# Kernel tuning notes

Hardware: AMD Instinct MI355X
Metric: run time of the kernel (lower is better)

The kernel has to match this reference:

```python
import jax, jax.numpy as jnp
import numpy as np

K, D, O, B = 65536, 256, 256, 1024

def setup_inputs() -> dict:
    key = jax.random.key(0)
    k1, k2, k3 = jax.random.split(key, 3)
    return {
        "x": jax.random.normal(k1, (B, D), dtype=jnp.float32),
        "mean": jax.random.normal(k2, (K, D), dtype=jnp.float32),
        "stddev": jnp.ones((K, D), dtype=jnp.float32),
        "outputs": jax.random.normal(k3, (K, O), dtype=jnp.float32),
        "top_k": 32,
    }

def reference(x, mean, stddev, outputs, top_k):
    # Joint Gaussian log-prob summed over feature dim, computed without the
    # [B, K, D] broadcast torch materializes. Expanding sum_d ((x-mu)/sigma)^2
    # gives three GEMM-shaped terms.
    d = x.shape[-1]
    inv_var = 1.0 / (stddev * stddev)                      # [K, D]
    quad = ((x * x) @ inv_var.T                            # [B, K]
            - 2.0 * (x @ (mean * inv_var).T)
            + jnp.sum(mean * mean * inv_var, axis=-1))
    log_norm = jnp.sum(jnp.log(stddev), axis=-1) + 0.5 * d * jnp.log(2.0 * jnp.pi)
    joint_lp = -0.5 * quad - log_norm                      # [B, K]
    top_lp, top_idx = jax.lax.top_k(joint_lp, top_k)       # [B, top_k]
    weights = jax.nn.softmax(top_lp, axis=-1)              # [B, top_k]
    gathered = outputs[top_idx]                            # [B, top_k, O]
    return jnp.einsum('bko,bk->bo', gathered, weights)     # [B, O]
```

## Files before the change

kernel.cpp:

```cpp
#include <hip/hip_runtime.h>
#include <stdint.h>

#define KCOMP 65536
#define DDIM  256
#define ODIM  256
#define BROWS 1024
#define NCB   512
#define NBLK  1024
#define LOG2PI_TERM 235.2482645f

typedef float f32x4 __attribute__((ext_vector_type(4)));
typedef __bf16 bf16x8 __attribute__((ext_vector_type(8)));
typedef unsigned int u32;
typedef unsigned long long u64;
typedef unsigned short u16;

typedef __attribute__((address_space(1))) const u32 gconst_u32;
typedef __attribute__((address_space(3))) u32 lds_u32;

__device__ __forceinline__ u16 f2bf(float f) {
  u32 b = __float_as_uint(f);
  b += 0x7FFFu + ((b >> 16) & 1u);
  return (u16)(b >> 16);
}
__device__ __forceinline__ u32 fkey(float f) {
  u32 b = __float_as_uint(f);
  return b ^ ((b >> 31) ? 0xFFFFFFFFu : 0x80000000u);
}

#define DPP_ROR1 0x121
#define DPP_ROR2 0x122
#define DPP_ROR4 0x124
#define DPP_ROR8 0x128

#define WS_A     0
#define WS_W     (1u << 20)
#define WS_CONST (WS_W + (64u << 20))
#define WS_KEY   (WS_CONST + (256u << 10))

__global__ void prep_A(const float* __restrict__ x, u16* __restrict__ A) {
  int l = threadIdx.x & 63;
  int wv = threadIdx.x >> 6;
  int t = blockIdx.x;
  int row = t * 16 + (l & 15);
  for (int u = 0; u < 4; ++u) {
    int cc = wv * 4 + u;
    int d0 = cc * 16 + ((l >> 4) << 2);
    float4 xv = *(const float4*)(x + (size_t)row * DDIM + d0);
    float xs[4] = {xv.x, xv.y, xv.z, xv.w};
    uint4 v;
    u32 wds[4];
    for (int e = 0; e < 4; ++e)
      wds[e] = (u32)f2bf(xs[e] * xs[e]) | ((u32)f2bf(-2.0f * xs[e]) << 16);
    v.x = wds[0]; v.y = wds[1]; v.z = wds[2]; v.w = wds[3];
    *(uint4*)(A + ((size_t)(t * 16 + cc) * 64 + l) * 8) = v;
  }
}

__global__ __launch_bounds__(256)
void prep_W(const float* __restrict__ mean, const float* __restrict__ stdd,
            u16* __restrict__ W, float* __restrict__ ck) {
  __shared__ u32 ldsW[4][16][268];
  int l = threadIdx.x & 63;
  int wv = threadIdx.x >> 6;
  int g = blockIdx.x * 4 + wv;
  for (int p = 0; p < 16; ++p) {
    int comp = g * 16 + p;
    float4 m4 = *(const float4*)(mean + (size_t)comp * DDIM + l * 4);
    float4 s4 = *(const float4*)(stdd + (size_t)comp * DDIM + l * 4);
    float ms[4] = {m4.x, m4.y, m4.z, m4.w};
    float ss[4] = {s4.x, s4.y, s4.z, s4.w};
    u32 wds[4];
    float gsum = 0.f;
    for (int e = 0; e < 4; ++e) {
      float iv = 1.0f / (ss[e] * ss[e]);
      float miv = ms[e] * iv;
      wds[e] = (u32)f2bf(iv) | ((u32)f2bf(miv) << 16);
      gsum += -0.5f * ms[e] * miv - __logf(ss[e]);
    }
    for (int d = 1; d < 64; d <<= 1) gsum += __shfl_xor(gsum, d);
    if (l == 0) ck[comp] = gsum - LOG2PI_TERM;
    uint4 v; v.x = wds[0]; v.y = wds[1]; v.z = wds[2]; v.w = wds[3];
    *(uint4*)&ldsW[wv][p][l * 4] = v;
  }
  __syncthreads();
  for (int cc = 0; cc < 16; ++cc) {
    uint4 v = *(const uint4*)&ldsW[wv][l & 15][cc * 16 + ((l >> 4) << 2)];
    *(uint4*)(W + ((size_t)(g * 16 + cc) * 64 + l) * 8) = v;
  }
}

__global__ __launch_bounds__(256, 2)
void main_gemm(const u16* __restrict__ A_ws, const u16* __restrict__ W_ws,
               const float* __restrict__ ck, u32* __restrict__ ckey) {
  __shared__ u16 Ash[2][16][512];
  __shared__ u32 wsel[2][16][9];
  int tid = threadIdx.x, l = tid & 63, w = tid >> 6;
  int nb = blockIdx.x & (NCB - 1);
  int rh = blockIdx.x >> 9;
  int g0 = nb * 8 + w * 2;

  bf16x8 wfA[16], wfB[16];
#pragma unroll
  for (int cc = 0; cc < 16; ++cc) {
    wfA[cc] = *(const bf16x8*)(W_ws + ((size_t)(g0 * 16 + cc) * 64 + l) * 8);
    wfB[cc] = *(const bf16x8*)(W_ws + ((size_t)((g0 + 1) * 16 + cc) * 64 + l) * 8);
  }
  float mycA = ck[g0 * 16 + (l & 15)];
  float mycB = ck[(g0 + 1) * 16 + (l & 15)];
  u32 cA = (u32)(w * 32 + (l & 15));
  u32 cB = cA + 16;

#define ISSUE(S, B)                                                           \
  {                                                                           \
    _Pragma("unroll")                                                         \
    for (int u = 0; u < 4; ++u) {                                             \
      int cell = w * 4 + u;                                                   \
      const u16* gsrc = A_ws +                                                \
        ((size_t)(rh * 32 + (S)) * 16 + cell) * 512 + (size_t)l * 8;          \
      __builtin_amdgcn_global_load_lds((gconst_u32*)gsrc,                     \
          (lds_u32*)&Ash[B][cell][0], 16, 0, 0);                              \
    }                                                                         \
  }

#define MERGE_EMIT(ST, B)                                                     \
  {                                                                           \
    int r = tid;                                                              \
    u32 top[4] = {~0u, ~0u, ~0u, ~0u};                                        \
    _Pragma("unroll")                                                         \
    for (int j = 0; j < 8; ++j) {                                             \
      u32 key = wsel[B][r][j];                                                \
      if (key < top[3]) {                                                     \
        top[3] = key;                                                         \
        for (int z = 3; z > 0 && top[z] < top[z - 1]; --z) {                  \
          u32 tt = top[z]; top[z] = top[z - 1]; top[z - 1] = tt;              \
        }                                                                     \
      }                                                                       \
    }                                                                         \
    int rowg = rh * 512 + (ST) * 16 + r;                                      \
    uint4 ov; ov.x = ~top[0]; ov.y = ~top[1]; ov.z = ~top[2]; ov.w = ~top[3]; \
    *(uint4*)&ckey[((size_t)rowg * NCB + nb) * 4] = ov;                       \
  }

  ISSUE(0, 0)
  for (int s = 0; s < 32; ++s) {
    int p = s & 1;
    __syncthreads();
    if (s < 31) ISSUE(s + 1, p ^ 1)
    if (s > 0 && tid < 16) MERGE_EMIT(s - 1, p ^ 1)

    f32x4 aA = (f32x4){0.f, 0.f, 0.f, 0.f};
    f32x4 aB = (f32x4){0.f, 0.f, 0.f, 0.f};
#pragma unroll
    for (int cc = 0; cc < 16; ++cc) {
      bf16x8 a = *(const bf16x8*)(&Ash[p][cc][(size_t)l * 8]);
      aA = __builtin_amdgcn_mfma_f32_16x16x32_bf16(a, wfA[cc], aA, 0, 0, 0);
      aB = __builtin_amdgcn_mfma_f32_16x16x32_bf16(a, wfB[cc], aB, 0, 0, 0);
    }

#pragma unroll
    for (int i = 0; i < 4; ++i) {
      float sA = fmaf(aA[i], -0.5f, mycA);
      float sB = fmaf(aB[i], -0.5f, mycB);
      u32 kA = (__float_as_uint(sA) & 0xFFFFFF00u) | cA;
      u32 kB = (__float_as_uint(sB) & 0xFFFFFF00u) | cB;
      u32 m1 = kA < kB ? kA : kB;
      u32 m2 = kA < kB ? kB : kA;
#define DSTEP(CTRL)                                                           \
      {                                                                       \
        u32 o1 = (u32)__builtin_amdgcn_mov_dpp((int)m1, CTRL, 0xf, 0xf, false); \
        u32 o2 = (u32)__builtin_amdgcn_mov_dpp((int)m2, CTRL, 0xf, 0xf, false); \
        u32 lo = m1 < o1 ? m1 : o1;                                           \
        u32 hi = m1 < o1 ? o1 : m1;                                           \
        u32 mn = m2 < o2 ? m2 : o2;                                           \
        m2 = hi < mn ? hi : mn;                                               \
        m1 = lo;                                                              \
      }
      DSTEP(DPP_ROR1) DSTEP(DPP_ROR2) DSTEP(DPP_ROR4) DSTEP(DPP_ROR8)
#undef DSTEP
      int r = ((l >> 4) << 2) + i;
      if ((l & 15) == 0) wsel[p][r][w * 2] = m1;
      else if ((l & 15) == 1) wsel[p][r][w * 2 + 1] = m2;
    }
  }
  __syncthreads();
  if (tid < 16) MERGE_EMIT(31, 1)
#undef ISSUE
#undef MERGE_EMIT
}

__global__ __launch_bounds__(256)
void finalize(const float* __restrict__ x, const float* __restrict__ mean,
              const float* __restrict__ stdd, const float* __restrict__ outs,
              const u32* __restrict__ ckey, float* __restrict__ out) {
  __shared__ u32 cksh[2048];
  __shared__ float xr[256];
  __shared__ float part[256];
  __shared__ int selk[64];
  __shared__ float ew[32];
  __shared__ int kf[32];
  __shared__ float invs_sh;
  int tid = threadIdx.x, l = tid & 63, v = tid >> 6;
  int row = blockIdx.x;

  for (int i = tid; i < 2048; i += 256)
    cksh[i] = ckey[(size_t)row * 2048 + i];
  xr[tid] = x[(size_t)row * DDIM + tid];
  __syncthreads();

#define REDUCE_MAX(m)                                                         \
  {                                                                           \
    u32 o;                                                                    \
    o = (u32)__builtin_amdgcn_mov_dpp((int)m, DPP_ROR1, 0xf, 0xf, false);     \
    m = m > o ? m : o;                                                        \
    o = (u32)__builtin_amdgcn_mov_dpp((int)m, DPP_ROR2, 0xf, 0xf, false);     \
    m = m > o ? m : o;                                                        \
    o = (u32)__builtin_amdgcn_mov_dpp((int)m, DPP_ROR4, 0xf, 0xf, false);     \
    m = m > o ? m : o;                                                        \
    o = (u32)__builtin_amdgcn_mov_dpp((int)m, DPP_ROR8, 0xf, 0xf, false);     \
    m = m > o ? m : o;                                                        \
    o = (u32)__shfl_xor((int)m, 16); m = m > o ? m : o;                       \
    o = (u32)__shfl_xor((int)m, 32); m = m > o ? m : o;                       \
  }

  {
    u32 ext[8];
#pragma unroll
    for (int i = 0; i < 8; ++i) {
      int j = v * 512 + i * 64 + l;
      ext[i] = (cksh[j] & 0xFFFFFE00u) | ((u32)l << 3) | (u32)i;
    }
#define CSW(a, b) { if (ext[a] < ext[b]) { u32 t = ext[a]; ext[a] = ext[b]; ext[b] = t; } }
    CSW(0,1) CSW(2,3) CSW(4,5) CSW(6,7)
    CSW(0,2) CSW(1,3) CSW(4,6) CSW(5,7)
    CSW(1,2) CSW(5,6)
    CSW(0,4) CSW(1,5) CSW(2,6) CSW(3,7)
    CSW(2,4) CSW(3,5)
    CSW(1,2) CSW(3,4) CSW(5,6)
#undef CSW
    for (int it = 0; it < 16; ++it) {
      u32 m = ext[0];
      REDUCE_MAX(m)
      if (m == ext[0]) {
#pragma unroll
        for (int z = 0; z < 7; ++z) ext[z] = ext[z + 1];
        ext[7] = 0;
      }
      if (l == 0) {
        int wl = (int)((m >> 3) & 63u), wi = (int)(m & 7u);
        int j = v * 512 + wi * 64 + wl;
        selk[v * 16 + it] = (int)((u32)(j >> 2) * 128u + (~cksh[j] & 0x7Fu));
      }
    }
  }
  __syncthreads();

  {
    int j = tid >> 2, q = tid & 3;
    int k = selk[j];
    const float* mr = mean + (size_t)k * DDIM + q * 64;
    const float* sr = stdd + (size_t)k * DDIM + q * 64;
    float s2 = 0.f, ls = 0.f;
    for (int i = 0; i < 16; ++i) {
      float4 m4 = *(const float4*)(mr + 4 * i);
      float4 s4 = *(const float4*)(sr + 4 * i);
      float4 x4 = *(const float4*)(&xr[q * 64 + 4 * i]);
      { float is = 1.f / s4.x; float df = (x4.x - m4.x) * is; s2 += df * df; ls += __logf(s4.x); }
      { float is = 1.f / s4.y; float df = (x4.y - m4.y) * is; s2 += df * df; ls += __logf(s4.y); }
      { float is = 1.f / s4.z; float df = (x4.z - m4.z) * is; s2 += df * df; ls += __logf(s4.z); }
      { float is = 1.f / s4.w; float df = (x4.w - m4.w) * is; s2 += df * df; ls += __logf(s4.w); }
    }
    part[tid] = -0.5f * s2 - ls;
  }
  __syncthreads();

  if (tid < 64) {
    float lp0 = part[l * 4] + part[l * 4 + 1] + part[l * 4 + 2] +
                part[l * 4 + 3] - LOG2PI_TERM;
    u32 ext = (fkey(lp0) & 0xFFFFFFC0u) | (u32)l;
    float maxlp = 0.f, ssum = 0.f;
    for (int it = 0; it < 32; ++it) {
      u32 m = ext;
      REDUCE_MAX(m)
      int j = (int)(m & 63u);
      u32 vb = m & 0xFFFFFFC0u;
      vb ^= (vb >> 31) ? 0x80000000u : 0xFFFFFFFFu;
      float lp = __uint_as_float(vb);
      if (it == 0) maxlp = lp;
      float e = __expf(lp - maxlp);
      ssum += e;
      if (l == 0) { ew[it] = e; kf[it] = selk[j]; }
      if (j == l) ext = 0;
    }
    if (l == 0) invs_sh = 1.0f / ssum;
  }
  __syncthreads();
#undef REDUCE_MAX

  {
    float a = 0.f;
    for (int i = 0; i < 32; ++i)
      a += ew[i] * outs[(size_t)kf[i] * ODIM + tid];
    out[(size_t)row * ODIM + tid] = a * invs_sh;
  }
}

extern "C" void kernel_launch(void* const* d_in, const int* in_sizes, int n_in,
                              void* d_out, int out_size, void* d_ws, size_t ws_size,
                              hipStream_t stream) {
  const float* x = (const float*)d_in[0];
  const float* mean = (const float*)d_in[1];
  const float* stdd = (const float*)d_in[2];
  const float* outs = (const float*)d_in[3];
  char* ws = (char*)d_ws;
  u16* A_ws = (u16*)(ws + WS_A);
  u16* W_ws = (u16*)(ws + WS_W);
  float* ck = (float*)(ws + WS_CONST);
  u32* ckey = (u32*)(ws + WS_KEY);

  prep_A<<<64, 256, 0, stream>>>(x, A_ws);
  prep_W<<<1024, 256, 0, stream>>>(mean, stdd, W_ws, ck);
  main_gemm<<<NBLK, 256, 0, stream>>>(A_ws, W_ws, ck, ckey);
  finalize<<<BROWS, 256, 0, stream>>>(x, mean, stdd, outs, ckey,
                                      (float*)d_out);
}
```

Baseline: 419.6 us.

## Fuse weight preprocessing into main GEMM and double row tile per stage

Removes the separate prep_W kernel and the bf16 weight workspace. Each main_gemm block now reads mean and stddev directly, builds its bf16 interleaved weight fragments and per-component constants through an LDS scratch area, then runs the GEMM. This avoids writing the intermediate weight buffer and reading it back, at the cost of each component's mean/stddev being read and converted by both row-half blocks. The pipeline also processes 32 rows per stage over 16 stages instead of 16 rows over 32, reusing each weight fragment across two A tiles. That raises LDS use to about 66 KB per block, which may limit occupancy.

```diff
diff --git a/kernel.cpp b/kernel.cpp
--- a/kernel.cpp
+++ b/kernel.cpp
@@ -34,9 +34,7 @@
 #define DPP_ROR8 0x128
 
 #define WS_A     0
-#define WS_W     (1u << 20)
-#define WS_CONST (WS_W + (64u << 20))
-#define WS_KEY   (WS_CONST + (256u << 10))
+#define WS_KEY   (1u << 20)
 
 __global__ void prep_A(const float* __restrict__ x, u16* __restrict__ A) {
   int l = threadIdx.x & 63;
@@ -57,69 +55,68 @@
   }
 }
 
-__global__ __launch_bounds__(256)
-void prep_W(const float* __restrict__ mean, const float* __restrict__ stdd,
-            u16* __restrict__ W, float* __restrict__ ck) {
-  __shared__ u32 ldsW[4][16][268];
-  int l = threadIdx.x & 63;
-  int wv = threadIdx.x >> 6;
-  int g = blockIdx.x * 4 + wv;
-  for (int p = 0; p < 16; ++p) {
-    int comp = g * 16 + p;
-    float4 m4 = *(const float4*)(mean + (size_t)comp * DDIM + l * 4);
-    float4 s4 = *(const float4*)(stdd + (size_t)comp * DDIM + l * 4);
-    float ms[4] = {m4.x, m4.y, m4.z, m4.w};
-    float ss[4] = {s4.x, s4.y, s4.z, s4.w};
-    u32 wds[4];
-    float gsum = 0.f;
-    for (int e = 0; e < 4; ++e) {
-      float iv = 1.0f / (ss[e] * ss[e]);
-      float miv = ms[e] * iv;
-      wds[e] = (u32)f2bf(iv) | ((u32)f2bf(miv) << 16);
-      gsum += -0.5f * ms[e] * miv - __logf(ss[e]);
-    }
-    for (int d = 1; d < 64; d <<= 1) gsum += __shfl_xor(gsum, d);
-    if (l == 0) ck[comp] = gsum - LOG2PI_TERM;
-    uint4 v; v.x = wds[0]; v.y = wds[1]; v.z = wds[2]; v.w = wds[3];
-    *(uint4*)&ldsW[wv][p][l * 4] = v;
-  }
-  __syncthreads();
-  for (int cc = 0; cc < 16; ++cc) {
-    uint4 v = *(const uint4*)&ldsW[wv][l & 15][cc * 16 + ((l >> 4) << 2)];
-    *(uint4*)(W + ((size_t)(g * 16 + cc) * 64 + l) * 8) = v;
-  }
-}
-
 __global__ __launch_bounds__(256, 2)
-void main_gemm(const u16* __restrict__ A_ws, const u16* __restrict__ W_ws,
-               const float* __restrict__ ck, u32* __restrict__ ckey) {
-  __shared__ u16 Ash[2][16][512];
-  __shared__ u32 wsel[2][16][9];
+void main_gemm(const u16* __restrict__ A_ws, const float* __restrict__ mean,
+               const float* __restrict__ stdd, u32* __restrict__ ckey) {
+  __shared__ __align__(16) char lds_raw[66560];
+  __shared__ u32 wsel[2][32][9];
   int tid = threadIdx.x, l = tid & 63, w = tid >> 6;
   int nb = blockIdx.x & (NCB - 1);
   int rh = blockIdx.x >> 9;
   int g0 = nb * 8 + w * 2;
-
-  bf16x8 wfA[16], wfB[16];
-#pragma unroll
-  for (int cc = 0; cc < 16; ++cc) {
-    wfA[cc] = *(const bf16x8*)(W_ws + ((size_t)(g0 * 16 + cc) * 64 + l) * 8);
-    wfB[cc] = *(const bf16x8*)(W_ws + ((size_t)((g0 + 1) * 16 + cc) * 64 + l) * 8);
-  }
-  float mycA = ck[g0 * 16 + (l & 15)];
-  float mycB = ck[(g0 + 1) * 16 + (l & 15)];
-  u32 cA = (u32)(w * 32 + (l & 15));
+  int p = l & 15, q = l >> 4;
+
+  bf16x8 wf[2][16];
+  float myc[2];
+  {
+    u32* scr = (u32*)(lds_raw + w * 16640);
+#pragma unroll
+    for (int gs = 0; gs < 2; ++gs) {
+      int comp = (g0 + gs) * 16 + p;
+      const float* mrow = mean + (size_t)comp * DDIM + q * 64;
+      const float* srow = stdd + (size_t)comp * DDIM + q * 64;
+      float gsum = 0.f;
+#pragma unroll
+      for (int i = 0; i < 16; ++i) {
+        float4 m4 = *(const float4*)(mrow + 4 * i);
+        float4 s4 = *(const float4*)(srow + 4 * i);
+        float ms[4] = {m4.x, m4.y, m4.z, m4.w};
+        float ss[4] = {s4.x, s4.y, s4.z, s4.w};
+        u32 wd[4];
+#pragma unroll
+        for (int e = 0; e < 4; ++e) {
+          float iv = __builtin_amdgcn_rcpf(ss[e] * ss[e]);
+          float miv = ms[e] * iv;
+          wd[e] = (u32)f2bf(iv) | ((u32)f2bf(miv) << 16);
+          gsum -= 0.5f * ms[e] * miv + __logf(ss[e]);
+        }
+        uint4 v; v.x = wd[0]; v.y = wd[1]; v.z = wd[2]; v.w = wd[3];
+        *(uint4*)(scr + p * 260 + q * 64 + i * 4) = v;
+      }
+      gsum += __shfl_xor(gsum, 16);
+      gsum += __shfl_xor(gsum, 32);
+      myc[gs] = gsum - LOG2PI_TERM;
+#pragma unroll
+      for (int cc = 0; cc < 16; ++cc)
+        wf[gs][cc] = *(const bf16x8*)(scr + p * 260 + cc * 16 + q * 4);
+    }
+  }
+  __syncthreads();
+
+  u32 cA = (u32)(w * 32 + p);
   u32 cB = cA + 16;
+#define ASHP(B, CELL) (lds_raw + ((size_t)(B) * 32 + (CELL)) * 1024)
 
 #define ISSUE(S, B)                                                           \
   {                                                                           \
     _Pragma("unroll")                                                         \
-    for (int u = 0; u < 4; ++u) {                                             \
-      int cell = w * 4 + u;                                                   \
+    for (int u = 0; u < 8; ++u) {                                             \
+      int cell = w * 8 + u;                                                   \
       const u16* gsrc = A_ws +                                                \
-        ((size_t)(rh * 32 + (S)) * 16 + cell) * 512 + (size_t)l * 8;          \
+        ((size_t)(rh * 32 + (S) * 2 + (cell >> 4)) * 16 + (cell & 15)) * 512  \
+        + (size_t)l * 8;                                                      \
       __builtin_amdgcn_global_load_lds((gconst_u32*)gsrc,                     \
-          (lds_u32*)&Ash[B][cell][0], 16, 0, 0);                              \
+          (lds_u32*)ASHP(B, cell), 16, 0, 0);                                 \
     }                                                                         \
   }
 
@@ -137,56 +134,66 @@
         }                                                                     \
       }                                                                       \
     }                                                                         \
-    int rowg = rh * 512 + (ST) * 16 + r;                                      \
+    int rowg = rh * 512 + (ST) * 32 + r;                                      \
     uint4 ov; ov.x = ~top[0]; ov.y = ~top[1]; ov.z = ~top[2]; ov.w = ~top[3]; \
     *(uint4*)&ckey[((size_t)rowg * NCB + nb) * 4] = ov;                       \
   }
 
   ISSUE(0, 0)
-  for (int s = 0; s < 32; ++s) {
-    int p = s & 1;
+  for (int s = 0; s < 16; ++s) {
+    int pb = s & 1;
     __syncthreads();
-    if (s < 31) ISSUE(s + 1, p ^ 1)
-    if (s > 0 && tid < 16) MERGE_EMIT(s - 1, p ^ 1)
-
-    f32x4 aA = (f32x4){0.f, 0.f, 0.f, 0.f};
-    f32x4 aB = (f32x4){0.f, 0.f, 0.f, 0.f};
+    if (s < 15) ISSUE(s + 1, pb ^ 1)
+    if (s > 0 && tid < 32) MERGE_EMIT(s - 1, pb ^ 1)
+
+    f32x4 ac[2][2];
+#pragma unroll
+    for (int t = 0; t < 2; ++t) {
+      ac[t][0] = (f32x4){0.f, 0.f, 0.f, 0.f};
+      ac[t][1] = (f32x4){0.f, 0.f, 0.f, 0.f};
+    }
 #pragma unroll
     for (int cc = 0; cc < 16; ++cc) {
-      bf16x8 a = *(const bf16x8*)(&Ash[p][cc][(size_t)l * 8]);
-      aA = __builtin_amdgcn_mfma_f32_16x16x32_bf16(a, wfA[cc], aA, 0, 0, 0);
-      aB = __builtin_amdgcn_mfma_f32_16x16x32_bf16(a, wfB[cc], aB, 0, 0, 0);
-    }
-
-#pragma unroll
-    for (int i = 0; i < 4; ++i) {
-      float sA = fmaf(aA[i], -0.5f, mycA);
-      float sB = fmaf(aB[i], -0.5f, mycB);
-      u32 kA = (__float_as_uint(sA) & 0xFFFFFF00u) | cA;
-      u32 kB = (__float_as_uint(sB) & 0xFFFFFF00u) | cB;
-      u32 m1 = kA < kB ? kA : kB;
-      u32 m2 = kA < kB ? kB : kA;
+      bf16x8 a0 = *(const bf16x8*)(ASHP(pb, cc) + (size_t)l * 16);
+      bf16x8 a1 = *(const bf16x8*)(ASHP(pb, 16 + cc) + (size_t)l * 16);
+      ac[0][0] = __builtin_amdgcn_mfma_f32_16x16x32_bf16(a0, wf[0][cc], ac[0][0], 0, 0, 0);
+      ac[0][1] = __builtin_amdgcn_mfma_f32_16x16x32_bf16(a0, wf[1][cc], ac[0][1], 0, 0, 0);
+      ac[1][0] = __builtin_amdgcn_mfma_f32_16x16x32_bf16(a1, wf[0][cc], ac[1][0], 0, 0, 0);
+      ac[1][1] = __builtin_amdgcn_mfma_f32_16x16x32_bf16(a1, wf[1][cc], ac[1][1], 0, 0, 0);
+    }
+
+#pragma unroll
+    for (int t = 0; t < 2; ++t)
+#pragma unroll
+      for (int i = 0; i < 4; ++i) {
+        float sA = fmaf(ac[t][0][i], -0.5f, myc[0]);
+        float sB = fmaf(ac[t][1][i], -0.5f, myc[1]);
+        u32 kA = (__float_as_uint(sA) & 0xFFFFFF00u) | cA;
+        u32 kB = (__float_as_uint(sB) & 0xFFFFFF00u) | cB;
+        u32 m1 = kA < kB ? kA : kB;
+        u32 m2 = kA < kB ? kB : kA;
 #define DSTEP(CTRL)                                                           \
-      {                                                                       \
-        u32 o1 = (u32)__builtin_amdgcn_mov_dpp((int)m1, CTRL, 0xf, 0xf, false); \
-        u32 o2 = (u32)__builtin_amdgcn_mov_dpp((int)m2, CTRL, 0xf, 0xf, false); \
-        u32 lo = m1 < o1 ? m1 : o1;                                           \
-        u32 hi = m1 < o1 ? o1 : m1;                                           \
-        u32 mn = m2 < o2 ? m2 : o2;                                           \
-        m2 = hi < mn ? hi : mn;                                               \
-        m1 = lo;                                                              \
+        {                                                                     \
+          u32 o1 = (u32)__builtin_amdgcn_mov_dpp((int)m1, CTRL, 0xf, 0xf, false); \
+          u32 o2 = (u32)__builtin_amdgcn_mov_dpp((int)m2, CTRL, 0xf, 0xf, false); \
+          u32 lo = m1 < o1 ? m1 : o1;                                         \
+          u32 hi = m1 < o1 ? o1 : m1;                                         \
+          u32 mn = m2 < o2 ? m2 : o2;                                         \
+          m2 = hi < mn ? hi : mn;                                             \
+          m1 = lo;                                                            \
+        }
+        DSTEP(DPP_ROR1) DSTEP(DPP_ROR2) DSTEP(DPP_ROR4) DSTEP(DPP_ROR8)
+#undef DSTEP
+        int r = t * 16 + q * 4 + i;
+        if (p == 0) wsel[pb][r][w * 2] = m1;
+        else if (p == 1) wsel[pb][r][w * 2 + 1] = m2;
       }
-      DSTEP(DPP_ROR1) DSTEP(DPP_ROR2) DSTEP(DPP_ROR4) DSTEP(DPP_ROR8)
-#undef DSTEP
-      int r = ((l >> 4) << 2) + i;
-      if ((l & 15) == 0) wsel[p][r][w * 2] = m1;
-      else if ((l & 15) == 1) wsel[p][r][w * 2 + 1] = m2;
-    }
-  }
-  __syncthreads();
-  if (tid < 16) MERGE_EMIT(31, 1)
+  }
+  __syncthreads();
+  if (tid < 32) MERGE_EMIT(15, 1)
 #undef ISSUE
 #undef MERGE_EMIT
+#undef ASHP
 }
 
 __global__ __launch_bounds__(256)
@@ -256,15 +263,15 @@
   __syncthreads();
 
   {
-    int j = tid >> 2, q = tid & 3;
+    int j = tid >> 2, qq = tid & 3;
     int k = selk[j];
-    const float* mr = mean + (size_t)k * DDIM + q * 64;
-    const float* sr = stdd + (size_t)k * DDIM + q * 64;
+    const float* mr = mean + (size_t)k * DDIM + qq * 64;
+    const float* sr = stdd + (size_t)k * DDIM + qq * 64;
     float s2 = 0.f, ls = 0.f;
     for (int i = 0; i < 16; ++i) {
       float4 m4 = *(const float4*)(mr + 4 * i);
       float4 s4 = *(const float4*)(sr + 4 * i);
-      float4 x4 = *(const float4*)(&xr[q * 64 + 4 * i]);
+      float4 x4 = *(const float4*)(&xr[qq * 64 + 4 * i]);
       { float is = 1.f / s4.x; float df = (x4.x - m4.x) * is; s2 += df * df; ls += __logf(s4.x); }
       { float is = 1.f / s4.y; float df = (x4.y - m4.y) * is; s2 += df * df; ls += __logf(s4.y); }
       { float is = 1.f / s4.z; float df = (x4.z - m4.z) * is; s2 += df * df; ls += __logf(s4.z); }
@@ -314,13 +321,10 @@
   const float* outs = (const float*)d_in[3];
   char* ws = (char*)d_ws;
   u16* A_ws = (u16*)(ws + WS_A);
-  u16* W_ws = (u16*)(ws + WS_W);
-  float* ck = (float*)(ws + WS_CONST);
   u32* ckey = (u32*)(ws + WS_KEY);
 
   prep_A<<<64, 256, 0, stream>>>(x, A_ws);
-  prep_W<<<1024, 256, 0, stream>>>(mean, stdd, W_ws, ck);
-  main_gemm<<<NBLK, 256, 0, stream>>>(A_ws, W_ws, ck, ckey);
+  main_gemm<<<NBLK, 256, 0, stream>>>(A_ws, mean, stdd, ckey);
   finalize<<<BROWS, 256, 0, stream>>>(x, mean, stdd, outs, ckey,
                                       (float*)d_out);
 }
```

Result: no change. 415.8 us (-0.9%).
